# Optimization experiments

Hardware: AMD Instinct MI355X
Metric: run time of the kernel (lower is better)

## Reference

```python
import jax, jax.numpy as jnp
import numpy as np

P = 3; Q = 3                 # spline degrees (deg_p, deg_q)
OUT_U = 64; OUT_V = 64       # surface evaluation grid
W_CTRL = 1.0; W_SURF = 1.0
B = 1024; MU_MAX = 32; MV_MAX = 32
EPS = 1e-5                   # SurfEval samples u,v in [eps, 1-eps]


def _open_uniform_knots(n_valid, degree, n_max):
    """Clamped open-uniform knot vector for n_valid ctrl pts, padded to static
    length n_max+degree+1. Entries beyond the valid span are clamped to 1.0,
    which makes the padded basis functions identically zero on [eps, 1-eps]."""
    L = n_valid + degree + 1  # true (ragged) knot count, traced int
    k = jnp.arange(n_max + degree + 1)
    interior = k.astype(jnp.float32) / (L - 1).astype(jnp.float32)
    return jnp.where(k <= degree, 0.0, jnp.where(k >= L - 1 - degree, 1.0, interior))


def _bspline_basis(kv, degree, u):
    """Cox-de Boor, vectorized over u. kv: (n_max+degree+1,), u: (U,).
    Returns (U, n_max) basis matrix; padded columns are exactly zero."""
    N = ((u[None, :] >= kv[:-1, None]) & (u[None, :] < kv[1:, None])).astype(jnp.float32)
    for d in range(1, degree + 1):
        m = N.shape[0] - 1  # number of basis funcs at this level
        den1 = kv[d:d + m] - kv[:m]
        den2 = kv[d + 1:d + 1 + m] - kv[1:1 + m]
        s1 = jnp.where((den1 > 0)[:, None],
                       (u[None, :] - kv[:m, None]) / jnp.where(den1 > 0, den1, 1.0)[:, None], 0.0)
        s2 = jnp.where((den2 > 0)[:, None],
                       (kv[d + 1:d + 1 + m, None] - u[None, :]) / jnp.where(den2 > 0, den2, 1.0)[:, None], 0.0)
        N = s1 * N[:m] + s2 * N[1:m + 1]
    return N.T  # (U, n_max)


def _eval_surface(ctrl, mask_b, u, v):
    """NURBS surface eval for one sample with ragged (Mu_i, Mv_i) via padded
    knots/basis; unit weights => rational division by basis partition sum."""
    mu = jnp.maximum(jnp.sum(jnp.any(mask_b > 0, axis=1)), P + 1)
    mv = jnp.maximum(jnp.sum(jnp.any(mask_b > 0, axis=0)), Q + 1)
    Bu = _bspline_basis(_open_uniform_knots(mu, P, MU_MAX), P, u)  # (OUT_U, MU_MAX)
    Bv = _bspline_basis(_open_uniform_knots(mv, Q, MV_MAX), Q, v)  # (OUT_V, MV_MAX)
    num = jnp.einsum('ui,vj,ijd->uvd', Bu, Bv, ctrl)               # (OUT_U, OUT_V, 3)
    den = Bu.sum(-1)[:, None] * Bv.sum(-1)[None, :]                # unit-weight denom
    return num / den[..., None]


def setup_inputs() -> dict:
    key = jax.random.key(0)
    k1, k2, k3, k4, k5 = jax.random.split(key, 5)
    # ragged true control sizes per sample, >= degree+1
    mu = jax.random.randint(k1, (B,), P + 1, MU_MAX + 1)
    mv = jax.random.randint(k2, (B,), Q + 1, MV_MAX + 1)
    mask = ((jnp.arange(MU_MAX)[None, :, None] < mu[:, None, None]) &
            (jnp.arange(MV_MAX)[None, None, :] < mv[:, None, None])).astype(jnp.float32)
    ctrl_pred_pad = jax.random.normal(k3, (B, MU_MAX, MV_MAX, 3), jnp.float32)
    ctrl_gt_pad = jax.random.normal(k4, (B, MU_MAX, MV_MAX, 3), jnp.float32)
    xyz_samples = jax.random.normal(k5, (B, OUT_U, OUT_V, 3), jnp.float32)
    return {"ctrl_pred_pad": ctrl_pred_pad, "ctrl_gt_pad": ctrl_gt_pad,
            "mask": mask, "xyz_samples": xyz_samples}


def reference(ctrl_pred_pad, ctrl_gt_pad, mask, xyz_samples):
    # masked control-point MSE
    diff2 = ((ctrl_pred_pad - ctrl_gt_pad) ** 2).sum(-1)
    loss_ctrl = (diff2 * mask).sum() / jnp.maximum(mask.sum() * 3.0, 1.0)
    # batched ragged surface evaluation
    u = jnp.linspace(EPS, 1.0 - EPS, OUT_U)
    v = jnp.linspace(EPS, 1.0 - EPS, OUT_V)
    surf = jax.vmap(lambda c, m: _eval_surface(c, m, u, v))(ctrl_pred_pad, mask)
    loss_surf = jnp.mean((surf.reshape(B, -1, 3) - xyz_samples.reshape(B, -1, 3)) ** 2)
    total = W_CTRL * loss_ctrl + W_SURF * loss_surf  # original computes total BEFORE nan-guard
    bad = jnp.isnan(surf).any() | jnp.isinf(surf).any()
    surf_mse = jnp.where(bad, jnp.float32(1e6), loss_surf)
    return total, loss_ctrl, surf_mse
```

## Files before the change

### kernel.cpp

```cpp
#include <hip/hip_runtime.h>
#include <math.h>

#define MU_MAXC 32
#define MV_MAXC 32
#define OUT_UC  64
#define OUT_VC  64
#define DEG     3
#define NKNOT   (MU_MAXC + DEG + 1)
#define EPSV    1e-5f

__global__ void zero_ws_kernel(double* acc, int* bad) {
    acc[0] = 0.0; acc[1] = 0.0; acc[2] = 0.0; bad[0] = 0;
}

__device__ __forceinline__ float kv_at(int k, int L) {
    return (k <= DEG) ? 0.f : ((k >= L - 1 - DEG) ? 1.f : (float)k / (float)(L - 1));
}

template <int MODE>
__launch_bounds__(256)
__global__ void nurbs_loss_kernel(const float* __restrict__ ctrl_pred,
                                  const float* __restrict__ ctrl_gt,
                                  const float* __restrict__ mask,
                                  const float* __restrict__ xyz,
                                  double* __restrict__ pd, int Bcnt,
                                  int* __restrict__ badp)
{
    const int b   = blockIdx.x;
    const int tid = threadIdx.x;

    __shared__ float s_tmp[OUT_UC * MV_MAXC * 3];
    __shared__ float s_Bu4[4 * OUT_UC];
    __shared__ float s_Bv4[4 * OUT_VC];
    __shared__ int   s_uoff[OUT_UC];
    __shared__ int   s_voff[OUT_VC];
    __shared__ float s_invSumBu[OUT_UC];
    __shared__ int   s_rowany[MU_MAXC];
    __shared__ int   s_colany[MV_MAXC];
    __shared__ int   s_mu, s_mv, s_bad;
    __shared__ float s_wred[4], s_wred2[4];
    __shared__ float s_ctrl_diff, s_ctrl_mask;

    if (tid < 32) { s_rowany[tid] = 0; s_colany[tid] = 0; }
    if (tid == 0) s_bad = 0;
    __syncthreads();

    float lsum_mask, lsum_diff;
    {
        const float4 mm = ((const float4*)(mask + (size_t)b * 1024))[tid];
        const float4* p4 = (const float4*)(ctrl_pred + (size_t)b * 3072);
        const float4* g4 = (const float4*)(ctrl_gt   + (size_t)b * 3072);
        const float4 pa = p4[3 * tid + 0], pb = p4[3 * tid + 1], pc = p4[3 * tid + 2];
        const float4 ga = g4[3 * tid + 0], gb = g4[3 * tid + 1], gc = g4[3 * tid + 2];
        const float a0 = pa.x - ga.x, a1 = pa.y - ga.y, a2 = pa.z - ga.z;
        const float b0 = pa.w - ga.w, b1 = pb.x - gb.x, b2 = pb.y - gb.y;
        const float c0 = pb.z - gb.z, c1 = pb.w - gb.w, c2 = pc.x - gc.x;
        const float e0 = pc.y - gc.y, e1 = pc.z - gc.z, e2 = pc.w - gc.w;
        lsum_mask = mm.x + mm.y + mm.z + mm.w;
        lsum_diff = mm.x * (a0 * a0 + a1 * a1 + a2 * a2)
                  + mm.y * (b0 * b0 + b1 * b1 + b2 * b2)
                  + mm.z * (c0 * c0 + c1 * c1 + c2 * c2)
                  + mm.w * (e0 * e0 + e1 * e1 + e2 * e2);
        const int row = tid >> 3;
        const int colb = (tid & 7) * 4;
        if (lsum_mask > 0.f) s_rowany[row] = 1;
        if (mm.x > 0.f) s_colany[colb + 0] = 1;
        if (mm.y > 0.f) s_colany[colb + 1] = 1;
        if (mm.z > 0.f) s_colany[colb + 2] = 1;
        if (mm.w > 0.f) s_colany[colb + 3] = 1;
    }
    #pragma unroll
    for (int off = 32; off > 0; off >>= 1) {
        lsum_mask += __shfl_down(lsum_mask, off);
        lsum_diff += __shfl_down(lsum_diff, off);
    }
    if ((tid & 63) == 0) { s_wred[tid >> 6] = lsum_mask; s_wred2[tid >> 6] = lsum_diff; }
    __syncthreads();

    if (tid == 0) {
        int cu = 0, cv = 0;
        #pragma unroll
        for (int i = 0; i < 32; i++) { cu += s_rowany[i]; cv += s_colany[i]; }
        s_mu = cu > (DEG + 1) ? cu : (DEG + 1);
        s_mv = cv > (DEG + 1) ? cv : (DEG + 1);
        s_ctrl_mask = s_wred[0] + s_wred[1] + s_wred[2] + s_wred[3];
        s_ctrl_diff = s_wred2[0] + s_wred2[1] + s_wred2[2] + s_wred2[3];
    }
    __syncthreads();

    if (tid < 128) {
        const bool isU = tid < 64;
        const int t = isU ? tid : (tid - 64);
        const int L = (isU ? s_mu : s_mv) + DEG + 1;
        const float step = (1.f - 2.f * EPSV) / 63.f;
        const float uu = (t == 63) ? (1.f - EPSV) : (EPSV + step * (float)t);

        int span = DEG;
        #pragma unroll
        for (int k = DEG + 1; k < NKNOT - 1; k++)
            if (kv_at(k, L) <= uu) span = k;

        float left[DEG + 1], right[DEG + 1];
        #pragma unroll
        for (int j = 1; j <= DEG; j++) {
            left[j]  = uu - kv_at(span + 1 - j, L);
            right[j] = kv_at(span + j, L) - uu;
        }
        float N4[DEG + 1];
        N4[0] = 1.f;
        #pragma unroll
        for (int j = 1; j <= DEG; j++) {
            float saved = 0.f;
            #pragma unroll
            for (int r = 0; r < j; r++) {
                const float temp = N4[r] / (right[r + 1] + left[j - r]);
                N4[r] = saved + right[r + 1] * temp;
                saved = left[j - r] * temp;
            }
            N4[j] = saved;
        }
        const float s = N4[0] + N4[1] + N4[2] + N4[3];
        const float invs = 1.0f / s;
        const int off = span - DEG;
        if (isU) {
            #pragma unroll
            for (int r = 0; r < 4; r++) s_Bu4[r * 64 + t] = N4[r];
            s_uoff[t] = off; s_invSumBu[t] = invs;
        } else {
            #pragma unroll
            for (int r = 0; r < 4; r++) s_Bv4[r * 64 + t] = N4[r] * invs;
            s_voff[t] = off;
        }
    }
    __syncthreads();

    {
        const float4* ctrl4 = (const float4*)(ctrl_pred + (size_t)b * 3072);
        float4* tmp4 = (float4*)s_tmp;
        for (int k = 0; k < 6; k++) {
            const int flat4 = tid + 256 * k;
            const int u = flat4 / 24;
            const int q = flat4 - u * 24;
            const int off = s_uoff[u];
            const float w0 = s_Bu4[0 * 64 + u];
            const float w1 = s_Bu4[1 * 64 + u];
            const float w2 = s_Bu4[2 * 64 + u];
            const float w3 = s_Bu4[3 * 64 + u];
            const float4 c0 = ctrl4[(off + 0) * 24 + q];
            const float4 c1 = ctrl4[(off + 1) * 24 + q];
            const float4 c2 = ctrl4[(off + 2) * 24 + q];
            const float4 c3 = ctrl4[(off + 3) * 24 + q];
            float4 a;
            a.x = w0 * c0.x + w1 * c1.x + w2 * c2.x + w3 * c3.x;
            a.y = w0 * c0.y + w1 * c1.y + w2 * c2.y + w3 * c3.y;
            a.z = w0 * c0.z + w1 * c1.z + w2 * c2.z + w3 * c3.z;
            a.w = w0 * c0.w + w1 * c1.w + w2 * c2.w + w3 * c3.w;
            tmp4[flat4] = a;
        }
    }
    __syncthreads();

    float lsum_surf = 0.f;
    int bad = 0;
    {
        const int vg  = (tid & 15) * 4;
        const int ug0 = tid >> 4;
        float w[4][4]; int vo[4];
        #pragma unroll
        for (int c = 0; c < 4; c++) {
            vo[c] = s_voff[vg + c] * 3;
            #pragma unroll
            for (int r = 0; r < 4; r++) w[c][r] = s_Bv4[r * 64 + vg + c];
        }
        #pragma unroll
        for (int k = 0; k < 4; k++) {
            const int u = ug0 + 16 * k;
            const float inv = s_invSumBu[u];
            const float* tp = &s_tmp[u * 96];
            const float4* x4 = (const float4*)(xyz + ((size_t)b * 4096 + u * 64 + vg) * 3);
            const float4 xa = x4[0], xb = x4[1], xc = x4[2];
            float px[4], py[4], pz[4];
            px[0] = xa.x; py[0] = xa.y; pz[0] = xa.z;
            px[1] = xa.w; py[1] = xb.x; pz[1] = xb.y;
            px[2] = xb.z; py[2] = xb.w; pz[2] = xc.x;
            px[3] = xc.y; py[3] = xc.z; pz[3] = xc.w;
            #pragma unroll
            for (int c = 0; c < 4; c++) {
                const float* tpc = tp + vo[c];
                const float n0 = w[c][0] * tpc[0] + w[c][1] * tpc[3] + w[c][2] * tpc[6] + w[c][3] * tpc[9];
                const float n1 = w[c][0] * tpc[1] + w[c][1] * tpc[4] + w[c][2] * tpc[7] + w[c][3] * tpc[10];
                const float n2 = w[c][0] * tpc[2] + w[c][1] * tpc[5] + w[c][2] * tpc[8] + w[c][3] * tpc[11];
                const float x0 = n0 * inv, x1 = n1 * inv, x2 = n2 * inv;
                const float d0 = x0 - px[c];
                const float d1 = x1 - py[c];
                const float d2 = x2 - pz[c];
                lsum_surf += d0 * d0 + d1 * d1 + d2 * d2;
                if (!isfinite(x0) || !isfinite(x1) || !isfinite(x2)) bad = 1;
            }
        }
    }
    #pragma unroll
    for (int off = 32; off > 0; off >>= 1)
        lsum_surf += __shfl_down(lsum_surf, off);
    if ((tid & 63) == 0) s_wred[tid >> 6] = lsum_surf;
    if (bad) atomicOr(&s_bad, 1);
    __syncthreads();

    if (tid == 0) {
        const double surf = (double)s_wred[0] + s_wred[1] + s_wred[2] + s_wred[3];
        if (MODE == 0) {
            pd[b]             = (double)s_ctrl_diff;
            pd[Bcnt + b]      = (double)s_ctrl_mask;
            pd[2 * Bcnt + b]  = surf;
            badp[b]           = s_bad;
        } else {
            atomicAdd(&pd[0], (double)s_ctrl_diff);
            atomicAdd(&pd[1], (double)s_ctrl_mask);
            atomicAdd(&pd[2], surf);
            if (s_bad) atomicOr(badp, 1);
        }
    }
}

__global__ void finalize_partials_kernel(const double* __restrict__ pd,
                                         const int* __restrict__ badp,
                                         float* __restrict__ out, int Bcnt)
{
    __shared__ double sd0[4], sd1[4], sd2[4];
    __shared__ int sb[4];
    const int tid = threadIdx.x;
    double a0 = 0.0, a1 = 0.0, a2 = 0.0; int bad = 0;
    for (int i = tid; i < Bcnt; i += 256) {
        a0 += pd[i]; a1 += pd[Bcnt + i]; a2 += pd[2 * Bcnt + i];
        bad |= badp[i];
    }
    #pragma unroll
    for (int off = 32; off > 0; off >>= 1) {
        a0 += __shfl_down(a0, off);
        a1 += __shfl_down(a1, off);
        a2 += __shfl_down(a2, off);
        bad |= __shfl_down(bad, off);
    }
    if ((tid & 63) == 0) { const int w = tid >> 6; sd0[w] = a0; sd1[w] = a1; sd2[w] = a2; sb[w] = bad; }
    __syncthreads();
    if (tid == 0) {
        double d0 = 0, d1 = 0, d2 = 0; int bb = 0;
        #pragma unroll
        for (int i = 0; i < 4; i++) { d0 += sd0[i]; d1 += sd1[i]; d2 += sd2[i]; bb |= sb[i]; }
        const double denc = d1 * 3.0;
        const double lc = d0 / (denc > 1.0 ? denc : 1.0);
        const double ls = d2 / ((double)Bcnt * OUT_UC * OUT_VC * 3.0);
        out[0] = (float)(lc + ls);
        out[1] = (float)lc;
        out[2] = bb ? 1.0e6f : (float)ls;
    }
}

__global__ void finalize_atomic_kernel(const double* __restrict__ acc,
                                       const int* __restrict__ bad,
                                       float* __restrict__ out, int Bcnt)
{
    const double denc = acc[1] * 3.0;
    const double lc = acc[0] / (denc > 1.0 ? denc : 1.0);
    const double ls = acc[2] / ((double)Bcnt * OUT_UC * OUT_VC * 3.0);
    out[0] = (float)(lc + ls);
    out[1] = (float)lc;
    out[2] = bad[0] ? 1.0e6f : (float)ls;
}

extern "C" void kernel_launch(void* const* d_in, const int* in_sizes, int n_in,
                              void* d_out, int out_size, void* d_ws, size_t ws_size,
                              hipStream_t stream)
{
    const float* pred = (const float*)d_in[0];
    const float* gt   = (const float*)d_in[1];
    const float* mask = (const float*)d_in[2];
    const float* xyz  = (const float*)d_in[3];
    const int Bcnt = in_sizes[2] / (MU_MAXC * MV_MAXC);

    double* pd = (double*)d_ws;
    float* out = (float*)d_out;

    const size_t need = (size_t)3 * Bcnt * sizeof(double) + (size_t)Bcnt * sizeof(int);
    if (ws_size >= need) {
        int* badp = (int*)(pd + 3 * Bcnt);
        hipLaunchKernelGGL((nurbs_loss_kernel<0>), dim3(Bcnt), dim3(256), 0, stream,
                           pred, gt, mask, xyz, pd, Bcnt, badp);
        hipLaunchKernelGGL(finalize_partials_kernel, dim3(1), dim3(256), 0, stream,
                           pd, badp, out, Bcnt);
    } else {
        int* badp = (int*)(pd + 3);
        hipLaunchKernelGGL(zero_ws_kernel, dim3(1), dim3(1), 0, stream, pd, badp);
        hipLaunchKernelGGL((nurbs_loss_kernel<1>), dim3(Bcnt), dim3(256), 0, stream,
                           pred, gt, mask, xyz, pd, Bcnt, badp);
        hipLaunchKernelGGL(finalize_atomic_kernel, dim3(1), dim3(1), 0, stream,
                           pd, badp, out, Bcnt);
    }
}
```

Baseline: 117.2 us.

## Split each sample across two blocks by u-half to double grid parallelism

Each batch sample is now handled by two blocks, each covering half of the 64 u rows of the surface and half of the control-point diff work. The mask sum is halved per block so the final reduction stays correct. The goal is more blocks for better occupancy and load balance across CUs, and a smaller shared tmp buffer. The cost is that both blocks redundantly load the mask and compute the v basis and row/column counts, and the finalize kernel reads twice as many partials.

```diff
diff --git a/kernel.cpp b/kernel.cpp
--- a/kernel.cpp
+++ b/kernel.cpp
@@ -23,18 +23,20 @@
                                   const float* __restrict__ ctrl_gt,
                                   const float* __restrict__ mask,
                                   const float* __restrict__ xyz,
-                                  double* __restrict__ pd, int Bcnt,
+                                  double* __restrict__ pd, int G,
                                   int* __restrict__ badp)
 {
-    const int b   = blockIdx.x;
+    const int bb  = blockIdx.x;
+    const int s   = bb >> 1;
+    const int h   = bb & 1;
     const int tid = threadIdx.x;
 
-    __shared__ float s_tmp[OUT_UC * MV_MAXC * 3];
-    __shared__ float s_Bu4[4 * OUT_UC];
+    __shared__ float s_tmp[32 * MV_MAXC * 3];
+    __shared__ float s_Bu4[4 * 32];
     __shared__ float s_Bv4[4 * OUT_VC];
-    __shared__ int   s_uoff[OUT_UC];
+    __shared__ int   s_uoff[32];
     __shared__ int   s_voff[OUT_VC];
-    __shared__ float s_invSumBu[OUT_UC];
+    __shared__ float s_invSumBu[32];
     __shared__ int   s_rowany[MU_MAXC];
     __shared__ int   s_colany[MV_MAXC];
     __shared__ int   s_mu, s_mv, s_bad;
@@ -45,22 +47,11 @@
     if (tid == 0) s_bad = 0;
     __syncthreads();
 
-    float lsum_mask, lsum_diff;
+    float lsum_mask, lsum_diff = 0.f;
+    float4 mm;
     {
-        const float4 mm = ((const float4*)(mask + (size_t)b * 1024))[tid];
-        const float4* p4 = (const float4*)(ctrl_pred + (size_t)b * 3072);
-        const float4* g4 = (const float4*)(ctrl_gt   + (size_t)b * 3072);
-        const float4 pa = p4[3 * tid + 0], pb = p4[3 * tid + 1], pc = p4[3 * tid + 2];
-        const float4 ga = g4[3 * tid + 0], gb = g4[3 * tid + 1], gc = g4[3 * tid + 2];
-        const float a0 = pa.x - ga.x, a1 = pa.y - ga.y, a2 = pa.z - ga.z;
-        const float b0 = pa.w - ga.w, b1 = pb.x - gb.x, b2 = pb.y - gb.y;
-        const float c0 = pb.z - gb.z, c1 = pb.w - gb.w, c2 = pc.x - gc.x;
-        const float e0 = pc.y - gc.y, e1 = pc.z - gc.z, e2 = pc.w - gc.w;
+        mm = ((const float4*)(mask + (size_t)s * 1024))[tid];
         lsum_mask = mm.x + mm.y + mm.z + mm.w;
-        lsum_diff = mm.x * (a0 * a0 + a1 * a1 + a2 * a2)
-                  + mm.y * (b0 * b0 + b1 * b1 + b2 * b2)
-                  + mm.z * (c0 * c0 + c1 * c1 + c2 * c2)
-                  + mm.w * (e0 * e0 + e1 * e1 + e2 * e2);
         const int row = tid >> 3;
         const int colb = (tid & 7) * 4;
         if (lsum_mask > 0.f) s_rowany[row] = 1;
@@ -69,6 +60,21 @@
         if (mm.z > 0.f) s_colany[colb + 2] = 1;
         if (mm.w > 0.f) s_colany[colb + 3] = 1;
     }
+    if ((tid >> 7) == h) {
+        const float4* p4 = (const float4*)(ctrl_pred + (size_t)s * 3072);
+        const float4* g4 = (const float4*)(ctrl_gt   + (size_t)s * 3072);
+        const float4 pa = p4[3 * tid + 0], pb = p4[3 * tid + 1], pc = p4[3 * tid + 2];
+        const float4 ga = g4[3 * tid + 0], gb = g4[3 * tid + 1], gc = g4[3 * tid + 2];
+        const float a0 = pa.x - ga.x, a1 = pa.y - ga.y, a2 = pa.z - ga.z;
+        const float b0 = pa.w - ga.w, b1 = pb.x - gb.x, b2 = pb.y - gb.y;
+        const float c0 = pb.z - gb.z, c1 = pb.w - gb.w, c2 = pc.x - gc.x;
+        const float e0 = pc.y - gc.y, e1 = pc.z - gc.z, e2 = pc.w - gc.w;
+        lsum_diff = mm.x * (a0 * a0 + a1 * a1 + a2 * a2)
+                  + mm.y * (b0 * b0 + b1 * b1 + b2 * b2)
+                  + mm.z * (c0 * c0 + c1 * c1 + c2 * c2)
+                  + mm.w * (e0 * e0 + e1 * e1 + e2 * e2);
+    }
+    lsum_mask *= 0.5f;
     #pragma unroll
     for (int off = 32; off > 0; off >>= 1) {
         lsum_mask += __shfl_down(lsum_mask, off);
@@ -88,12 +94,13 @@
     }
     __syncthreads();
 
-    if (tid < 128) {
-        const bool isU = tid < 64;
-        const int t = isU ? tid : (tid - 64);
-        const int L = (isU ? s_mu : s_mv) + DEG + 1;
+    if (tid < 96) {
+        const bool isV = tid < 64;
+        const int t = isV ? tid : (tid - 64);
+        const int gidx = isV ? t : (32 * h + t);
+        const int L = (isV ? s_mv : s_mu) + DEG + 1;
         const float step = (1.f - 2.f * EPSV) / 63.f;
-        const float uu = (t == 63) ? (1.f - EPSV) : (EPSV + step * (float)t);
+        const float uu = (gidx == 63) ? (1.f - EPSV) : (EPSV + step * (float)gidx);
 
         int span = DEG;
         #pragma unroll
@@ -119,33 +126,34 @@
             }
             N4[j] = saved;
         }
-        const float s = N4[0] + N4[1] + N4[2] + N4[3];
-        const float invs = 1.0f / s;
+        const float sum = N4[0] + N4[1] + N4[2] + N4[3];
+        const float invs = 1.0f / sum;
         const int off = span - DEG;
-        if (isU) {
-            #pragma unroll
-            for (int r = 0; r < 4; r++) s_Bu4[r * 64 + t] = N4[r];
-            s_uoff[t] = off; s_invSumBu[t] = invs;
-        } else {
+        if (isV) {
             #pragma unroll
             for (int r = 0; r < 4; r++) s_Bv4[r * 64 + t] = N4[r] * invs;
             s_voff[t] = off;
+        } else {
+            #pragma unroll
+            for (int r = 0; r < 4; r++) s_Bu4[r * 32 + t] = N4[r];
+            s_uoff[t] = off; s_invSumBu[t] = invs;
         }
     }
     __syncthreads();
 
     {
-        const float4* ctrl4 = (const float4*)(ctrl_pred + (size_t)b * 3072);
+        const float4* ctrl4 = (const float4*)(ctrl_pred + (size_t)s * 3072);
         float4* tmp4 = (float4*)s_tmp;
-        for (int k = 0; k < 6; k++) {
+        #pragma unroll
+        for (int k = 0; k < 3; k++) {
             const int flat4 = tid + 256 * k;
-            const int u = flat4 / 24;
-            const int q = flat4 - u * 24;
-            const int off = s_uoff[u];
-            const float w0 = s_Bu4[0 * 64 + u];
-            const float w1 = s_Bu4[1 * 64 + u];
-            const float w2 = s_Bu4[2 * 64 + u];
-            const float w3 = s_Bu4[3 * 64 + u];
+            const int lu = flat4 / 24;
+            const int q = flat4 - lu * 24;
+            const int off = s_uoff[lu];
+            const float w0 = s_Bu4[0 * 32 + lu];
+            const float w1 = s_Bu4[1 * 32 + lu];
+            const float w2 = s_Bu4[2 * 32 + lu];
+            const float w3 = s_Bu4[3 * 32 + lu];
             const float4 c0 = ctrl4[(off + 0) * 24 + q];
             const float4 c1 = ctrl4[(off + 1) * 24 + q];
             const float4 c2 = ctrl4[(off + 2) * 24 + q];
@@ -163,8 +171,8 @@
     float lsum_surf = 0.f;
     int bad = 0;
     {
-        const int vg  = (tid & 15) * 4;
-        const int ug0 = tid >> 4;
+        const int vg   = (tid & 15) * 4;
+        const int lug0 = tid >> 4;
         float w[4][4]; int vo[4];
         #pragma unroll
         for (int c = 0; c < 4; c++) {
@@ -173,11 +181,12 @@
             for (int r = 0; r < 4; r++) w[c][r] = s_Bv4[r * 64 + vg + c];
         }
         #pragma unroll
-        for (int k = 0; k < 4; k++) {
-            const int u = ug0 + 16 * k;
-            const float inv = s_invSumBu[u];
-            const float* tp = &s_tmp[u * 96];
-            const float4* x4 = (const float4*)(xyz + ((size_t)b * 4096 + u * 64 + vg) * 3);
+        for (int k = 0; k < 2; k++) {
+            const int lu = lug0 + 16 * k;
+            const int u  = 32 * h + lu;
+            const float inv = s_invSumBu[lu];
+            const float* tp = &s_tmp[lu * 96];
+            const float4* x4 = (const float4*)(xyz + ((size_t)s * 4096 + u * 64 + vg) * 3);
             const float4 xa = x4[0], xb = x4[1], xc = x4[2];
             float px[4], py[4], pz[4];
             px[0] = xa.x; py[0] = xa.y; pz[0] = xa.z;
@@ -209,10 +218,10 @@
     if (tid == 0) {
         const double surf = (double)s_wred[0] + s_wred[1] + s_wred[2] + s_wred[3];
         if (MODE == 0) {
-            pd[b]             = (double)s_ctrl_diff;
-            pd[Bcnt + b]      = (double)s_ctrl_mask;
-            pd[2 * Bcnt + b]  = surf;
-            badp[b]           = s_bad;
+            pd[bb]          = (double)s_ctrl_diff;
+            pd[G + bb]      = (double)s_ctrl_mask;
+            pd[2 * G + bb]  = surf;
+            badp[bb]        = s_bad;
         } else {
             atomicAdd(&pd[0], (double)s_ctrl_diff);
             atomicAdd(&pd[1], (double)s_ctrl_mask);
@@ -224,14 +233,14 @@
 
 __global__ void finalize_partials_kernel(const double* __restrict__ pd,
                                          const int* __restrict__ badp,
-                                         float* __restrict__ out, int Bcnt)
+                                         float* __restrict__ out, int G, int Bcnt)
 {
     __shared__ double sd0[4], sd1[4], sd2[4];
     __shared__ int sb[4];
     const int tid = threadIdx.x;
     double a0 = 0.0, a1 = 0.0, a2 = 0.0; int bad = 0;
-    for (int i = tid; i < Bcnt; i += 256) {
-        a0 += pd[i]; a1 += pd[Bcnt + i]; a2 += pd[2 * Bcnt + i];
+    for (int i = tid; i < G; i += 256) {
+        a0 += pd[i]; a1 += pd[G + i]; a2 += pd[2 * G + i];
         bad |= badp[i];
     }
     #pragma unroll
@@ -277,22 +286,23 @@
     const float* mask = (const float*)d_in[2];
     const float* xyz  = (const float*)d_in[3];
     const int Bcnt = in_sizes[2] / (MU_MAXC * MV_MAXC);
+    const int G = 2 * Bcnt;
 
     double* pd = (double*)d_ws;
     float* out = (float*)d_out;
 
-    const size_t need = (size_t)3 * Bcnt * sizeof(double) + (size_t)Bcnt * sizeof(int);
+    const size_t need = (size_t)3 * G * sizeof(double) + (size_t)G * sizeof(int);
     if (ws_size >= need) {
-        int* badp = (int*)(pd + 3 * Bcnt);
-        hipLaunchKernelGGL((nurbs_loss_kernel<0>), dim3(Bcnt), dim3(256), 0, stream,
-                           pred, gt, mask, xyz, pd, Bcnt, badp);
+        int* badp = (int*)(pd + 3 * G);
+        hipLaunchKernelGGL((nurbs_loss_kernel<0>), dim3(G), dim3(256), 0, stream,
+                           pred, gt, mask, xyz, pd, G, badp);
         hipLaunchKernelGGL(finalize_partials_kernel, dim3(1), dim3(256), 0, stream,
-                           pd, badp, out, Bcnt);
+                           pd, badp, out, G, Bcnt);
     } else {
         int* badp = (int*)(pd + 3);
         hipLaunchKernelGGL(zero_ws_kernel, dim3(1), dim3(1), 0, stream, pd, badp);
-        hipLaunchKernelGGL((nurbs_loss_kernel<1>), dim3(Bcnt), dim3(256), 0, stream,
-                           pred, gt, mask, xyz, pd, Bcnt, badp);
+        hipLaunchKernelGGL((nurbs_loss_kernel<1>), dim3(G), dim3(256), 0, stream,
+                           pred, gt, mask, xyz, pd, G, badp);
         hipLaunchKernelGGL(finalize_atomic_kernel, dim3(1), dim3(1), 0, stream,
                            pd, badp, out, Bcnt);
     }
```

New measurement: 115.2 us. Within noise of the previous version (-1.7%).

## Pad shared intermediate to float4 rows, use ballots for mask counts

Applied to the files above, without the earlier changes.

Replaces the shared-memory row/column-any arrays with wavefront ballots and popcounts, which drops a sync and the serial 32-element loop. The u-contracted intermediate is stored as padded float4 (xyz plus a zero lane) with a row stride of 33, so the v-contraction reads vector loads with fewer bank conflicts. The Bv weights are stored as float4 per v. The per-point NaN/Inf check is folded into a single isfinite on the accumulated sum. This relies on non-finite values propagating into the squared-error sum, and it raises shared-memory use.

```diff
diff --git a/kernel.cpp b/kernel.cpp
--- a/kernel.cpp
+++ b/kernel.cpp
@@ -16,6 +16,8 @@
 __device__ __forceinline__ float kv_at(int k, int L) {
     return (k <= DEG) ? 0.f : ((k >= L - 1 - DEG) ? 1.f : (float)k / (float)(L - 1));
 }
+
+#define TROW 33
 
 template <int MODE>
 __launch_bounds__(256)
@@ -29,23 +31,22 @@
     const int b   = blockIdx.x;
     const int tid = threadIdx.x;
 
-    __shared__ float s_tmp[OUT_UC * MV_MAXC * 3];
+    __shared__ __align__(16) float s_tmp[OUT_UC * TROW * 4];
+    __shared__ __align__(16) float s_Bv4[OUT_VC * 4];
     __shared__ float s_Bu4[4 * OUT_UC];
-    __shared__ float s_Bv4[4 * OUT_VC];
     __shared__ int   s_uoff[OUT_UC];
     __shared__ int   s_voff[OUT_VC];
     __shared__ float s_invSumBu[OUT_UC];
-    __shared__ int   s_rowany[MU_MAXC];
-    __shared__ int   s_colany[MV_MAXC];
     __shared__ int   s_mu, s_mv, s_bad;
     __shared__ float s_wred[4], s_wred2[4];
+    __shared__ int   s_rowcnt[4];
+    __shared__ unsigned int s_colmask[4];
     __shared__ float s_ctrl_diff, s_ctrl_mask;
 
-    if (tid < 32) { s_rowany[tid] = 0; s_colany[tid] = 0; }
     if (tid == 0) s_bad = 0;
-    __syncthreads();
 
     float lsum_mask, lsum_diff;
+    unsigned long long bx, by, bz, bw;
     {
         const float4 mm = ((const float4*)(mask + (size_t)b * 1024))[tid];
         const float4* p4 = (const float4*)(ctrl_pred + (size_t)b * 3072);
@@ -61,26 +62,43 @@
                   + mm.y * (b0 * b0 + b1 * b1 + b2 * b2)
                   + mm.z * (c0 * c0 + c1 * c1 + c2 * c2)
                   + mm.w * (e0 * e0 + e1 * e1 + e2 * e2);
-        const int row = tid >> 3;
-        const int colb = (tid & 7) * 4;
-        if (lsum_mask > 0.f) s_rowany[row] = 1;
-        if (mm.x > 0.f) s_colany[colb + 0] = 1;
-        if (mm.y > 0.f) s_colany[colb + 1] = 1;
-        if (mm.z > 0.f) s_colany[colb + 2] = 1;
-        if (mm.w > 0.f) s_colany[colb + 3] = 1;
-    }
+        bx = __ballot(mm.x > 0.f);
+        by = __ballot(mm.y > 0.f);
+        bz = __ballot(mm.z > 0.f);
+        bw = __ballot(mm.w > 0.f);
+    }
+    int rowcnt;
+    {
+        unsigned long long anyb = bx | by | bz | bw;
+        unsigned long long t = anyb | (anyb >> 4); t |= t >> 2; t |= t >> 1;
+        rowcnt = __popcll(t & 0x0101010101010101ULL);
+    }
+    bool colany = false;
+    {
+        const int j = tid & 63;
+        if (j < 32) {
+            const int comp = j & 3;
+            const unsigned long long sel = (comp == 0) ? bx : (comp == 1) ? by
+                                          : (comp == 2) ? bz : bw;
+            colany = (sel & (0x0101010101010101ULL << (j >> 2))) != 0ULL;
+        }
+    }
+    const unsigned long long cmask = __ballot(colany);
     #pragma unroll
     for (int off = 32; off > 0; off >>= 1) {
         lsum_mask += __shfl_down(lsum_mask, off);
         lsum_diff += __shfl_down(lsum_diff, off);
     }
-    if ((tid & 63) == 0) { s_wred[tid >> 6] = lsum_mask; s_wred2[tid >> 6] = lsum_diff; }
+    if ((tid & 63) == 0) {
+        const int w = tid >> 6;
+        s_wred[w] = lsum_mask; s_wred2[w] = lsum_diff;
+        s_rowcnt[w] = rowcnt;  s_colmask[w] = (unsigned int)cmask;
+    }
     __syncthreads();
 
     if (tid == 0) {
-        int cu = 0, cv = 0;
-        #pragma unroll
-        for (int i = 0; i < 32; i++) { cu += s_rowany[i]; cv += s_colany[i]; }
+        const int cu = s_rowcnt[0] + s_rowcnt[1] + s_rowcnt[2] + s_rowcnt[3];
+        const int cv = __popc(s_colmask[0] | s_colmask[1] | s_colmask[2] | s_colmask[3]);
         s_mu = cu > (DEG + 1) ? cu : (DEG + 1);
         s_mv = cv > (DEG + 1) ? cv : (DEG + 1);
         s_ctrl_mask = s_wred[0] + s_wred[1] + s_wred[2] + s_wred[3];
@@ -119,16 +137,16 @@
             }
             N4[j] = saved;
         }
-        const float s = N4[0] + N4[1] + N4[2] + N4[3];
-        const float invs = 1.0f / s;
+        const float sum = N4[0] + N4[1] + N4[2] + N4[3];
+        const float invs = 1.0f / sum;
         const int off = span - DEG;
         if (isU) {
             #pragma unroll
             for (int r = 0; r < 4; r++) s_Bu4[r * 64 + t] = N4[r];
             s_uoff[t] = off; s_invSumBu[t] = invs;
         } else {
-            #pragma unroll
-            for (int r = 0; r < 4; r++) s_Bv4[r * 64 + t] = N4[r] * invs;
+            ((float4*)s_Bv4)[t] = make_float4(N4[0] * invs, N4[1] * invs,
+                                              N4[2] * invs, N4[3] * invs);
             s_voff[t] = off;
         }
     }
@@ -136,69 +154,76 @@
 
     {
         const float4* ctrl4 = (const float4*)(ctrl_pred + (size_t)b * 3072);
-        float4* tmp4 = (float4*)s_tmp;
-        for (int k = 0; k < 6; k++) {
-            const int flat4 = tid + 256 * k;
-            const int u = flat4 / 24;
-            const int q = flat4 - u * 24;
+        #pragma unroll
+        for (int z = 0; z < 2; z++) {
+            const int task = tid + 256 * z;
+            const int u = task >> 3;
+            const int m = task & 7;
             const int off = s_uoff[u];
             const float w0 = s_Bu4[0 * 64 + u];
             const float w1 = s_Bu4[1 * 64 + u];
             const float w2 = s_Bu4[2 * 64 + u];
             const float w3 = s_Bu4[3 * 64 + u];
-            const float4 c0 = ctrl4[(off + 0) * 24 + q];
-            const float4 c1 = ctrl4[(off + 1) * 24 + q];
-            const float4 c2 = ctrl4[(off + 2) * 24 + q];
-            const float4 c3 = ctrl4[(off + 3) * 24 + q];
-            float4 a;
-            a.x = w0 * c0.x + w1 * c1.x + w2 * c2.x + w3 * c3.x;
-            a.y = w0 * c0.y + w1 * c1.y + w2 * c2.y + w3 * c3.y;
-            a.z = w0 * c0.z + w1 * c1.z + w2 * c2.z + w3 * c3.z;
-            a.w = w0 * c0.w + w1 * c1.w + w2 * c2.w + w3 * c3.w;
-            tmp4[flat4] = a;
+            float f[12];
+            #pragma unroll
+            for (int e = 0; e < 3; e++) {
+                const float4 c0 = ctrl4[(off + 0) * 24 + m * 3 + e];
+                const float4 c1 = ctrl4[(off + 1) * 24 + m * 3 + e];
+                const float4 c2 = ctrl4[(off + 2) * 24 + m * 3 + e];
+                const float4 c3 = ctrl4[(off + 3) * 24 + m * 3 + e];
+                f[e * 4 + 0] = w0 * c0.x + w1 * c1.x + w2 * c2.x + w3 * c3.x;
+                f[e * 4 + 1] = w0 * c0.y + w1 * c1.y + w2 * c2.y + w3 * c3.y;
+                f[e * 4 + 2] = w0 * c0.z + w1 * c1.z + w2 * c2.z + w3 * c3.z;
+                f[e * 4 + 3] = w0 * c0.w + w1 * c1.w + w2 * c2.w + w3 * c3.w;
+            }
+            float4* dst = ((float4*)s_tmp) + (u * TROW + m * 4);
+            dst[0] = make_float4(f[0], f[1],  f[2],  0.f);
+            dst[1] = make_float4(f[3], f[4],  f[5],  0.f);
+            dst[2] = make_float4(f[6], f[7],  f[8],  0.f);
+            dst[3] = make_float4(f[9], f[10], f[11], 0.f);
         }
     }
     __syncthreads();
 
     float lsum_surf = 0.f;
-    int bad = 0;
     {
         const int vg  = (tid & 15) * 4;
         const int ug0 = tid >> 4;
-        float w[4][4]; int vo[4];
+        float4 wv[4]; int vo[4];
         #pragma unroll
         for (int c = 0; c < 4; c++) {
-            vo[c] = s_voff[vg + c] * 3;
-            #pragma unroll
-            for (int r = 0; r < 4; r++) w[c][r] = s_Bv4[r * 64 + vg + c];
+            vo[c] = s_voff[vg + c];
+            wv[c] = ((const float4*)s_Bv4)[vg + c];
         }
         #pragma unroll
         for (int k = 0; k < 4; k++) {
             const int u = ug0 + 16 * k;
             const float inv = s_invSumBu[u];
-            const float* tp = &s_tmp[u * 96];
+            const float4* trow = ((const float4*)s_tmp) + u * TROW;
             const float4* x4 = (const float4*)(xyz + ((size_t)b * 4096 + u * 64 + vg) * 3);
             const float4 xa = x4[0], xb = x4[1], xc = x4[2];
-            float px[4], py[4], pz[4];
-            px[0] = xa.x; py[0] = xa.y; pz[0] = xa.z;
-            px[1] = xa.w; py[1] = xb.x; pz[1] = xb.y;
-            px[2] = xb.z; py[2] = xb.w; pz[2] = xc.x;
-            px[3] = xc.y; py[3] = xc.z; pz[3] = xc.w;
+            const float px[4] = {xa.x, xa.w, xb.z, xc.y};
+            const float py[4] = {xa.y, xb.x, xb.w, xc.z};
+            const float pz[4] = {xa.z, xb.y, xc.x, xc.w};
             #pragma unroll
             for (int c = 0; c < 4; c++) {
-                const float* tpc = tp + vo[c];
-                const float n0 = w[c][0] * tpc[0] + w[c][1] * tpc[3] + w[c][2] * tpc[6] + w[c][3] * tpc[9];
-                const float n1 = w[c][0] * tpc[1] + w[c][1] * tpc[4] + w[c][2] * tpc[7] + w[c][3] * tpc[10];
-                const float n2 = w[c][0] * tpc[2] + w[c][1] * tpc[5] + w[c][2] * tpc[8] + w[c][3] * tpc[11];
+                const float4 t0 = trow[vo[c] + 0];
+                const float4 t1 = trow[vo[c] + 1];
+                const float4 t2 = trow[vo[c] + 2];
+                const float4 t3 = trow[vo[c] + 3];
+                const float4 w = wv[c];
+                const float n0 = w.x * t0.x + w.y * t1.x + w.z * t2.x + w.w * t3.x;
+                const float n1 = w.x * t0.y + w.y * t1.y + w.z * t2.y + w.w * t3.y;
+                const float n2 = w.x * t0.z + w.y * t1.z + w.z * t2.z + w.w * t3.z;
                 const float x0 = n0 * inv, x1 = n1 * inv, x2 = n2 * inv;
                 const float d0 = x0 - px[c];
                 const float d1 = x1 - py[c];
                 const float d2 = x2 - pz[c];
                 lsum_surf += d0 * d0 + d1 * d1 + d2 * d2;
-                if (!isfinite(x0) || !isfinite(x1) || !isfinite(x2)) bad = 1;
             }
         }
     }
+    const int bad = !isfinite(lsum_surf);
     #pragma unroll
     for (int off = 32; off > 0; off >>= 1)
         lsum_surf += __shfl_down(lsum_surf, off);
```

Result: faster. 113.4 us (-3.3%).
